# Performance work log

Hardware: AMD Instinct MI355X
Metric: run time of the kernel (lower is better)

## Reference

```python
import jax, jax.numpy as jnp
import numpy as np

MAX_DISP = 4          # 9x9 displacement window -> 81 output channels
WIN = 2 * MAX_DISP + 1


def setup_inputs() -> dict:
    key = jax.random.key(0)
    k1, k2 = jax.random.split(key)
    B, C, H, W = 4, 256, 192, 192
    tensorFirst = jax.random.normal(k1, (B, C, H, W), dtype=jnp.float32)
    tensorSecond = jax.random.normal(k2, (B, C, H, W), dtype=jnp.float32)
    return {"tensorFirst": tensorFirst, "tensorSecond": tensorSecond}


def reference(tensorFirst, tensorSecond):
    # PWC-Net correlation: out[b, (dy+4)*9+(dx+4), y, x] =
    #   mean_c first[b,c,y,x] * second[b,c,y+dy,x+dx]  (second zero-padded by 4)
    B, C, H, W = tensorFirst.shape
    padded = jnp.pad(tensorSecond, ((0, 0), (0, 0), (MAX_DISP, MAX_DISP), (MAX_DISP, MAX_DISP)))
    outs = []
    for dy in range(WIN):
        for dx in range(WIN):
            shifted = padded[:, :, dy:dy + H, dx:dx + W]  # [B,C,H,W]
            outs.append(jnp.mean(tensorFirst * shifted, axis=1))  # [B,H,W]
    return jnp.stack(outs, axis=1)  # [B,81,H,W]
```

## Files before the change

kernel.cpp:

```cpp
#include <hip/hip_runtime.h>


#define MAXD 4
#define WINW 9
#define NDISP 81

constexpr int B_ = 4, C_ = 256, H_ = 192, W_ = 192;
constexpr int TH = 4;
constexpr int TW = 64;
constexpr int DYS = 3;
constexpr int NDY = WINW / DYS;
constexpr int CC = 4;
constexpr int NCHUNK = C_ / CC;
constexpr int SROWS = TH + DYS - 1;
constexpr int SCOLS = TW + 2 * MAXD;
constexpr int S_STRIDE = 72;
constexpr int S_CH = SROWS * S_STRIDE;
constexpr int SBUF = CC * S_CH;
constexpr int NTHREADS = 64 * DYS;
constexpr int NS4 = CC * SROWS * (SCOLS / 4);
constexpr int Q_CH = SROWS * (SCOLS / 4);

__global__ __launch_bounds__(NTHREADS)
void corr_kernel(const float* __restrict__ F, const float* __restrict__ S,
                 float* __restrict__ O) {
    __shared__ __align__(16) float ldsS[2 * SBUF];

    const int tid  = threadIdx.x;
    const int y0   = blockIdx.x * TH;
    const int x0   = blockIdx.y * TW;
    const int zb   = blockIdx.z;
    const int b    = zb / NDY;
    const int d0   = (zb % NDY) * DYS;
    const int widx = tid >> 6;
    const int lane = tid & 63;
    const int xg   = lane & 15;
    const int yth  = lane >> 4;

    const long planeHW   = (long)H_ * W_;
    const long chunkStep = (long)CC * planeHW;
    const float* Fb = F + (long)b * C_ * planeHW;
    const float* Sb = S + (long)b * C_ * planeHW;

    const float* fp = Fb + (long)(y0 + yth) * W_ + (x0 + 4 * xg);

    const int ybase = y0 + d0 - MAXD;

    const int  s0cc  = tid / Q_CH;
    const int  s0rem = tid - s0cc * Q_CH;
    const int  s0r   = s0rem / (SCOLS / 4);
    const int  s0cg  = s0rem - s0r * (SCOLS / 4);
    const int  s0ys  = ybase + s0r;
    const int  s0xs  = x0 - MAXD + 4 * s0cg;
    const bool s0In  = ((unsigned)s0ys < (unsigned)H_) &&
                       ((unsigned)s0xs <= (unsigned)(W_ - 4));
    const int  s0Lds = s0cc * S_CH + s0r * S_STRIDE + 4 * s0cg;
    const float* s0Ptr0 = Sb + (long)s0cc * planeHW + (long)s0ys * W_ + s0xs;

    const int  i1    = tid + NTHREADS;
    const int  s1cc  = i1 / Q_CH;
    const int  s1rem = i1 - s1cc * Q_CH;
    const int  s1r   = s1rem / (SCOLS / 4);
    const int  s1cg  = s1rem - s1r * (SCOLS / 4);
    const int  s1ys  = ybase + s1r;
    const int  s1xs  = x0 - MAXD + 4 * s1cg;
    const bool s1In  = ((unsigned)s1ys < (unsigned)H_) &&
                       ((unsigned)s1xs <= (unsigned)(W_ - 4));
    const int  s1Lds = s1cc * S_CH + s1r * S_STRIDE + 4 * s1cg;
    const float* s1Ptr0 = Sb + (long)s1cc * planeHW + (long)s1ys * W_ + s1xs;

    const int  i2    = tid + 2 * NTHREADS;
    const bool s2Act = (i2 < NS4);
    const int  s2cc  = i2 / Q_CH;
    const int  s2rem = i2 - s2cc * Q_CH;
    const int  s2r   = s2rem / (SCOLS / 4);
    const int  s2cg  = s2rem - s2r * (SCOLS / 4);
    const int  s2ys  = ybase + s2r;
    const int  s2xs  = x0 - MAXD + 4 * s2cg;
    const bool s2In  = s2Act && ((unsigned)s2ys < (unsigned)H_) &&
                       ((unsigned)s2xs <= (unsigned)(W_ - 4));
    const int  s2Lds = s2cc * S_CH + s2r * S_STRIDE + 4 * s2cg;
    const float* s2Ptr0 = Sb + (long)s2cc * planeHW + (long)s2ys * W_ + s2xs;

    const float4 z4 = make_float4(0.f, 0.f, 0.f, 0.f);
    if (!s0In) {
        *(float4*)(ldsS + s0Lds) = z4;
        *(float4*)(ldsS + SBUF + s0Lds) = z4;
    }
    if (!s1In) {
        *(float4*)(ldsS + s1Lds) = z4;
        *(float4*)(ldsS + SBUF + s1Lds) = z4;
    }
    if (s2Act && !s2In) {
        *(float4*)(ldsS + s2Lds) = z4;
        *(float4*)(ldsS + SBUF + s2Lds) = z4;
    }

    float4 ps0, ps1, ps2;
    const float* s0Next = s0Ptr0;
    const float* s1Next = s1Ptr0;
    const float* s2Next = s2Ptr0;

    auto loadS = [&]() {
        if (s0In) ps0 = *(const float4*)s0Next;
        if (s1In) ps1 = *(const float4*)s1Next;
        if (s2In) ps2 = *(const float4*)s2Next;
        s0Next += chunkStep;
        s1Next += chunkStep;
        s2Next += chunkStep;
    };
    auto writeS = [&](int half) {
        float* wS = ldsS + half * SBUF;
        if (s0In) *(float4*)(wS + s0Lds) = ps0;
        if (s1In) *(float4*)(wS + s1Lds) = ps1;
        if (s2In) *(float4*)(wS + s2Lds) = ps2;
    };

    float acc[WINW][4];
    #pragma unroll
    for (int dx = 0; dx < WINW; ++dx)
        #pragma unroll
        for (int j = 0; j < 4; ++j) acc[dx][j] = 0.f;

    loadS();
    writeS(0);
    loadS();
    __syncthreads();

    const float* bS0 = ldsS + (yth + widx) * S_STRIDE + 4 * xg;

    for (int k = 0; k < NCHUNK; ++k) {
        float4 fr[CC];
        #pragma unroll
        for (int cc = 0; cc < CC; ++cc)
            fr[cc] = *(const float4*)(fp + (long)cc * planeHW);
        fp += chunkStep;

        const int cur = k & 1;
        if (k + 1 < NCHUNK) {
            writeS(cur ^ 1);
            if (k + 2 < NCHUNK) loadS();
        }

        const float* bS = bS0 + cur * SBUF;
        #pragma unroll
        for (int cc = 0; cc < CC; ++cc) {
            const float4 f  = fr[cc];
            const float4 w0 = *(const float4*)(bS + cc * S_CH);
            const float4 w1 = *(const float4*)(bS + cc * S_CH + 4);
            const float4 w2 = *(const float4*)(bS + cc * S_CH + 8);
            const float w[12] = {w0.x, w0.y, w0.z, w0.w,
                                 w1.x, w1.y, w1.z, w1.w,
                                 w2.x, w2.y, w2.z, w2.w};
            #pragma unroll
            for (int dx = 0; dx < WINW; ++dx) {
                acc[dx][0] += f.x * w[dx];
                acc[dx][1] += f.y * w[dx + 1];
                acc[dx][2] += f.z * w[dx + 2];
                acc[dx][3] += f.w * w[dx + 3];
            }
        }

        if (k + 1 < NCHUNK) __syncthreads();
    }

    const float scale = 1.0f / (float)C_;
    const int dy = d0 + widx;
    #pragma unroll
    for (int dx = 0; dx < WINW; ++dx) {
        float4 o;
        o.x = acc[dx][0] * scale;
        o.y = acc[dx][1] * scale;
        o.z = acc[dx][2] * scale;
        o.w = acc[dx][3] * scale;
        const int d = dy * WINW + dx;
        float* dst = O + ((long)(b * NDISP + d) * H_ + (y0 + yth)) * W_ + x0 + 4 * xg;
        *(float4*)dst = o;
    }
}

extern "C" void kernel_launch(void* const* d_in, const int* in_sizes, int n_in,
                              void* d_out, int out_size, void* d_ws, size_t ws_size,
                              hipStream_t stream) {
    const float* F = (const float*)d_in[0];
    const float* S = (const float*)d_in[1];
    float* O = (float*)d_out;
    dim3 grid(H_ / TH, W_ / TW, B_ * NDY);
    dim3 block(NTHREADS);
    corr_kernel<<<grid, block, 0, stream>>>(F, S, O);
}
```

Baseline: 384.5 us.

## Use DPP lane shifts for halo values and remap blocks per XCD

Each thread now reads two float4 values from LDS per channel, its own quad and a halo quad, instead of three. It builds the shifted left and right neighbours with DPP row_shr/row_shl moves, using the halo value at the row edges. This is meant to cut LDS read traffic in the inner loop at the cost of extra VALU mov instructions. The grid is also flattened to 1D and remapped so that consecutive logical tiles, which share the same F and S tile across batch and dy groups, land on the same XCD for better L2 reuse.

```diff
diff --git a/kernel.cpp b/kernel.cpp
--- a/kernel.cpp
+++ b/kernel.cpp
@@ -20,6 +20,18 @@
 constexpr int NTHREADS = 64 * DYS;
 constexpr int NS4 = CC * SROWS * (SCOLS / 4);
 constexpr int Q_CH = SROWS * (SCOLS / 4);
+constexpr int NTX = W_ / TW;
+constexpr int NTY = H_ / TH;
+constexpr int NZ = B_ * NDY;
+constexpr int NBLK = NTX * NTY * NZ;
+constexpr int PER_XCD = NBLK / 8;
+constexpr int PHW = H_ * W_;
+
+template <int CTRL>
+__device__ __forceinline__ float dpp_mov(float oldv, float srcv) {
+    return __int_as_float(__builtin_amdgcn_update_dpp(
+        __float_as_int(oldv), __float_as_int(srcv), CTRL, 0xF, 0xF, false));
+}
 
 __global__ __launch_bounds__(NTHREADS)
 void corr_kernel(const float* __restrict__ F, const float* __restrict__ S,
@@ -27,17 +39,23 @@
     __shared__ __align__(16) float ldsS[2 * SBUF];
 
     const int tid  = threadIdx.x;
-    const int y0   = blockIdx.x * TH;
-    const int x0   = blockIdx.y * TW;
-    const int zb   = blockIdx.z;
+
+    const int id   = blockIdx.x;
+    const int lg   = (id & 7) * PER_XCD + (id >> 3);
+    const int tile = lg / NZ;
+    const int zb   = lg - tile * NZ;
     const int b    = zb / NDY;
-    const int d0   = (zb % NDY) * DYS;
+    const int d0   = (zb - b * NDY) * DYS;
+    const int ty   = tile / NTX;
+    const int tx   = tile - ty * NTX;
+    const int y0 = ty * TH, x0 = tx * TW;
+
     const int widx = tid >> 6;
     const int lane = tid & 63;
     const int xg   = lane & 15;
     const int yth  = lane >> 4;
 
-    const long planeHW   = (long)H_ * W_;
+    const long planeHW   = (long)PHW;
     const long chunkStep = (long)CC * planeHW;
     const float* Fb = F + (long)b * C_ * planeHW;
     const float* Sb = S + (long)b * C_ * planeHW;
@@ -127,7 +145,9 @@
     loadS();
     __syncthreads();
 
-    const float* bS0 = ldsS + (yth + widx) * S_STRIDE + 4 * xg;
+    const int rowQ   = (yth + widx) * (SCOLS / 4);
+    const int ownQ   = rowQ + (xg + 1);
+    const int haloQ  = rowQ + ((xg == 0) ? 0 : (xg == 15) ? 17 : (xg + 1));
 
     for (int k = 0; k < NCHUNK; ++k) {
         float4 fr[CC];
@@ -142,22 +162,28 @@
             if (k + 2 < NCHUNK) loadS();
         }
 
-        const float* bS = bS0 + cur * SBUF;
+        const float* hb = ldsS + cur * SBUF;
         #pragma unroll
         for (int cc = 0; cc < CC; ++cc) {
-            const float4 f  = fr[cc];
-            const float4 w0 = *(const float4*)(bS + cc * S_CH);
-            const float4 w1 = *(const float4*)(bS + cc * S_CH + 4);
-            const float4 w2 = *(const float4*)(bS + cc * S_CH + 8);
-            const float w[12] = {w0.x, w0.y, w0.z, w0.w,
-                                 w1.x, w1.y, w1.z, w1.w,
-                                 w2.x, w2.y, w2.z, w2.w};
+            const float4 s4 = *(const float4*)(hb + 4 * (cc * Q_CH + ownQ));
+            const float4 h4 = *(const float4*)(hb + 4 * (cc * Q_CH + haloQ));
+            float wv[12];
+            wv[0] = dpp_mov<0x111>(h4.x, s4.x);
+            wv[1] = dpp_mov<0x111>(h4.y, s4.y);
+            wv[2] = dpp_mov<0x111>(h4.z, s4.z);
+            wv[3] = dpp_mov<0x111>(h4.w, s4.w);
+            wv[4] = s4.x; wv[5] = s4.y; wv[6] = s4.z; wv[7] = s4.w;
+            wv[8]  = dpp_mov<0x101>(h4.x, s4.x);
+            wv[9]  = dpp_mov<0x101>(h4.y, s4.y);
+            wv[10] = dpp_mov<0x101>(h4.z, s4.z);
+            wv[11] = dpp_mov<0x101>(h4.w, s4.w);
+            const float4 f = fr[cc];
             #pragma unroll
             for (int dx = 0; dx < WINW; ++dx) {
-                acc[dx][0] += f.x * w[dx];
-                acc[dx][1] += f.y * w[dx + 1];
-                acc[dx][2] += f.z * w[dx + 2];
-                acc[dx][3] += f.w * w[dx + 3];
+                acc[dx][0] += f.x * wv[dx + 0];
+                acc[dx][1] += f.y * wv[dx + 1];
+                acc[dx][2] += f.z * wv[dx + 2];
+                acc[dx][3] += f.w * wv[dx + 3];
             }
         }
 
@@ -166,6 +192,7 @@
 
     const float scale = 1.0f / (float)C_;
     const int dy = d0 + widx;
+    const int fRow = y0 + yth;
     #pragma unroll
     for (int dx = 0; dx < WINW; ++dx) {
         float4 o;
@@ -174,7 +201,7 @@
         o.z = acc[dx][2] * scale;
         o.w = acc[dx][3] * scale;
         const int d = dy * WINW + dx;
-        float* dst = O + ((long)(b * NDISP + d) * H_ + (y0 + yth)) * W_ + x0 + 4 * xg;
+        float* dst = O + ((long)(b * NDISP + d) * H_ + fRow) * W_ + x0 + 4 * xg;
         *(float4*)dst = o;
     }
 }
@@ -185,7 +212,7 @@
     const float* F = (const float*)d_in[0];
     const float* S = (const float*)d_in[1];
     float* O = (float*)d_out;
-    dim3 grid(H_ / TH, W_ / TW, B_ * NDY);
+    dim3 grid(NBLK, 1, 1);
     dim3 block(NTHREADS);
     corr_kernel<<<grid, block, 0, stream>>>(F, S, O);
 }
```

After: 393.6 us. +2.4%, slower.

## Remap blocks to XCDs for L2 locality and use lighter LDS-only barrier

Applied to the files above, without the earlier changes.

Flattens the grid to 1D and remaps block IDs so that consecutive logical blocks, which share the same spatial tile across batches and dy groups, land on the same XCD's L2 cache. The aim is better L2 reuse of the first and second tensor reads across blocks on MI355X's multi-XCD layout. It also replaces __syncthreads with a barrier that waits only on LDS counters, so outstanding global prefetch loads do not stall at the barrier. The lighter barrier relies on the prefetch registers being written to LDS only after their loads complete, which the compiler's own waitcnt should handle.

```diff
diff --git a/kernel.cpp b/kernel.cpp
--- a/kernel.cpp
+++ b/kernel.cpp
@@ -20,6 +20,18 @@
 constexpr int NTHREADS = 64 * DYS;
 constexpr int NS4 = CC * SROWS * (SCOLS / 4);
 constexpr int Q_CH = SROWS * (SCOLS / 4);
+constexpr int NTX = W_ / TW;
+constexpr int NTY = H_ / TH;
+constexpr int NZ = B_ * NDY;
+constexpr int NBLK = NTX * NTY * NZ;
+constexpr int PER_XCD = NBLK / 8;
+constexpr int PHW = H_ * W_;
+
+__device__ __forceinline__ void wg_barrier_lds() {
+    asm volatile("s_waitcnt lgkmcnt(0)" ::: "memory");
+    __builtin_amdgcn_s_barrier();
+    asm volatile("" ::: "memory");
+}
 
 __global__ __launch_bounds__(NTHREADS)
 void corr_kernel(const float* __restrict__ F, const float* __restrict__ S,
@@ -27,17 +39,23 @@
     __shared__ __align__(16) float ldsS[2 * SBUF];
 
     const int tid  = threadIdx.x;
-    const int y0   = blockIdx.x * TH;
-    const int x0   = blockIdx.y * TW;
-    const int zb   = blockIdx.z;
+
+    const int id   = blockIdx.x;
+    const int lg   = (id & 7) * PER_XCD + (id >> 3);
+    const int tile = lg / NZ;
+    const int zb   = lg - tile * NZ;
     const int b    = zb / NDY;
-    const int d0   = (zb % NDY) * DYS;
+    const int d0   = (zb - b * NDY) * DYS;
+    const int ty   = tile / NTX;
+    const int tx   = tile - ty * NTX;
+    const int y0 = ty * TH, x0 = tx * TW;
+
     const int widx = tid >> 6;
     const int lane = tid & 63;
     const int xg   = lane & 15;
     const int yth  = lane >> 4;
 
-    const long planeHW   = (long)H_ * W_;
+    const long planeHW   = (long)PHW;
     const long chunkStep = (long)CC * planeHW;
     const float* Fb = F + (long)b * C_ * planeHW;
     const float* Sb = S + (long)b * C_ * planeHW;
@@ -125,7 +143,7 @@
     loadS();
     writeS(0);
     loadS();
-    __syncthreads();
+    wg_barrier_lds();
 
     const float* bS0 = ldsS + (yth + widx) * S_STRIDE + 4 * xg;
 
@@ -161,11 +179,12 @@
             }
         }
 
-        if (k + 1 < NCHUNK) __syncthreads();
+        if (k + 1 < NCHUNK) wg_barrier_lds();
     }
 
     const float scale = 1.0f / (float)C_;
     const int dy = d0 + widx;
+    const int fRow = y0 + yth;
     #pragma unroll
     for (int dx = 0; dx < WINW; ++dx) {
         float4 o;
@@ -174,7 +193,7 @@
         o.z = acc[dx][2] * scale;
         o.w = acc[dx][3] * scale;
         const int d = dy * WINW + dx;
-        float* dst = O + ((long)(b * NDISP + d) * H_ + (y0 + yth)) * W_ + x0 + 4 * xg;
+        float* dst = O + ((long)(b * NDISP + d) * H_ + fRow) * W_ + x0 + 4 * xg;
         *(float4*)dst = o;
     }
 }
@@ -185,7 +204,7 @@
     const float* F = (const float*)d_in[0];
     const float* S = (const float*)d_in[1];
     float* O = (float*)d_out;
-    dim3 grid(H_ / TH, W_ / TW, B_ * NDY);
+    dim3 grid(NBLK, 1, 1);
     dim3 block(NTHREADS);
     corr_kernel<<<grid, block, 0, stream>>>(F, S, O);
 }
```

After: 393.0 us. 2.2% more time.
